# Kernel tuning notes

Hardware: AMD Instinct MI355X
Metric: run time of the kernel (lower is better)

## Reference

```python
import jax, jax.numpy as jnp
import numpy as np

BER = 0.02          # ber_curve.ber_at(snr_db) evaluated at snr_db=10
BITS = 9            # ceil(log2(512)) for both coarse and fine codebooks
KC = 512
KF = 512
B, HC, WC, HF, WF, D = 64, 32, 32, 64, 64, 128


def _bitflip_channel(idx, u, bits, K):
    """Pack->bitflip->unpack->clip, vectorized.

    LSB-first packing of exactly bits-per-symbol means flipping bits of the
    packed byte stream == flipping each symbol's `bits` bits independently
    (flipped padding bits in the final byte are discarded by unpack).
    idx: [...] int32, u: [..., bits] float32 uniform(0,1).
    """
    shifts = jnp.arange(bits, dtype=jnp.int32)
    bitmat = (idx[..., None] >> shifts) & 1                       # [..., bits]
    flips = (u < BER).astype(jnp.int32)
    bitmat = jnp.bitwise_xor(bitmat, flips)
    rx = jnp.sum(bitmat << shifts, axis=-1)                       # [...]
    return jnp.clip(rx, 0, K - 1)


def setup_inputs() -> dict:
    key = jax.random.key(0)
    k1, k2, k3, k4, k5, k6 = jax.random.split(key, 6)
    return {
        "idx_c": jax.random.randint(k1, (B, HC, WC), 0, KC, dtype=jnp.int32),
        "idx_f": jax.random.randint(k2, (B, HF, WF), 0, KF, dtype=jnp.int32),
        "codebook_c": jax.random.normal(k3, (KC, D), dtype=jnp.float32),
        "codebook_f": jax.random.normal(k4, (KF, D), dtype=jnp.float32),
        "flip_u_c": jax.random.uniform(k5, (B, HC, WC, BITS), dtype=jnp.float32),
        "flip_u_f": jax.random.uniform(k6, (B, HF, WF, BITS), dtype=jnp.float32),
    }


def reference(idx_c, idx_f, codebook_c, codebook_f, flip_u_c, flip_u_f):
    rx_c = _bitflip_channel(idx_c, flip_u_c, BITS, KC)            # [B,Hc,Wc]
    rx_f = _bitflip_channel(idx_f, flip_u_f, BITS, KF)            # [B,Hf,Wf]
    # indices_to_quantized: embedding gather from each codebook
    q_coarse = codebook_c[rx_c]                                   # [B,Hc,Wc,D]
    q_fine = codebook_f[rx_f]                                     # [B,Hf,Wf,D]
    b = q_fine.shape[0]
    out = jnp.concatenate(
        [q_fine.reshape(b, -1), q_coarse.reshape(b, -1)], axis=1
    )
    return out
```

## Files before the change

kernel.cpp:

```cpp
#include <hip/hip_runtime.h>


constexpr int   BITS       = 9;
constexpr float BER        = 0.02f;
constexpr int   Bn         = 64;
constexpr int   HC = 32, WC = 32, HF = 64, WF = 64, D = 128;
constexpr int   NF         = Bn * HF * WF;
constexpr int   NC         = Bn * HC * WC;
constexpr int   NTOT       = NF + NC;
constexpr int   FINE_ROW   = HF * WF * D;
constexpr int   COARSE_ROW = HC * WC * D;
constexpr int   ROW        = FINE_ROW + COARSE_ROW;

__global__ __launch_bounds__(256) void flip_kernel(
    const int*   __restrict__ idx_c,
    const int*   __restrict__ idx_f,
    const float* __restrict__ u_c,
    const float* __restrict__ u_f,
    int*         __restrict__ rx)
{
    const int s = blockIdx.x * 256 + threadIdx.x;
    const float* u;  const int* idxp;  int local;
    if (s < NF) { u = u_f; idxp = idx_f; local = s; }
    else        { u = u_c; idxp = idx_c; local = s - NF; }
    const float* up = u + (size_t)local * BITS;
    int flip = 0;
    #pragma unroll
    for (int k = 0; k < BITS; ++k)
        flip |= (up[k] < BER) ? (1 << k) : 0;
    rx[s] = (idxp[local] ^ flip) & 511;
}

constexpr int GRID  = 2048;
constexpr int ITERS = NTOT / (8 * GRID);

__global__ __launch_bounds__(256) void gather_kernel(
    const float* __restrict__ cb_c,
    const float* __restrict__ cb_f,
    const int*   __restrict__ rx,
    float*       __restrict__ out)
{
    const int t          = threadIdx.x;
    const int sym_in_blk = t >> 5;
    const int lane32     = t & 31;

    #pragma unroll 2
    for (int it = 0; it < ITERS; ++it) {
        const int i = (it * GRID + blockIdx.x) * 8 + sym_in_blk;
        const int row = rx[i];

        const float* cb;  int off;
        if (i < NF) {
            const int b = i >> 12, rem = i & 4095;
            off = b * ROW + rem * D;                cb = cb_f;
        } else {
            const int j = i - NF;
            const int b = j >> 10, rem = j & 1023;
            off = b * ROW + FINE_ROW + rem * D;     cb = cb_c;
        }

        const float4 val = ((const float4*)(cb + row * D))[lane32];
        ((float4*)(out + off))[lane32] = val;
    }
}

extern "C" void kernel_launch(void* const* d_in, const int* in_sizes, int n_in,
                              void* d_out, int out_size, void* d_ws, size_t ws_size,
                              hipStream_t stream) {
    const int*   idx_c = (const int*)  d_in[0];
    const int*   idx_f = (const int*)  d_in[1];
    const float* cb_c  = (const float*)d_in[2];
    const float* cb_f  = (const float*)d_in[3];
    const float* u_c   = (const float*)d_in[4];
    const float* u_f   = (const float*)d_in[5];
    float*       out   = (float*)d_out;
    int*         rx    = (int*)d_ws;

    flip_kernel<<<NTOT / 256, 256, 0, stream>>>(idx_c, idx_f, u_c, u_f, rx);
    gather_kernel<<<GRID, 256, 0, stream>>>(cb_c, cb_f, rx, out);
}
```

Before: 184.5 us.

## Fuse bit-flip channel and codebook gather into one kernel via shared memory

Merges the flip kernel and the gather kernel into a single launch. Each block computes received indices and output offsets for its contiguous 160 symbols into shared memory, then gathers codebook rows. This removes the second kernel launch and the global round trip of the rx workspace. The cost is that only 160 of 256 threads do the flip phase before a barrier, so the strided u loads sit on the critical path of every block.

```diff
diff --git a/kernel.cpp b/kernel.cpp
--- a/kernel.cpp
+++ b/kernel.cpp
@@ -12,55 +12,60 @@
 constexpr int   COARSE_ROW = HC * WC * D;
 constexpr int   ROW        = FINE_ROW + COARSE_ROW;
 
-__global__ __launch_bounds__(256) void flip_kernel(
+constexpr int   GRID       = 2048;
+constexpr int   SPB        = NTOT / GRID;
+constexpr int   P2_ITERS   = SPB / 8;
+
+__global__ __launch_bounds__(256) void fused_chan_gather(
     const int*   __restrict__ idx_c,
     const int*   __restrict__ idx_f,
+    const float* __restrict__ cb_c,
+    const float* __restrict__ cb_f,
     const float* __restrict__ u_c,
     const float* __restrict__ u_f,
-    int*         __restrict__ rx)
-{
-    const int s = blockIdx.x * 256 + threadIdx.x;
-    const float* u;  const int* idxp;  int local;
-    if (s < NF) { u = u_f; idxp = idx_f; local = s; }
-    else        { u = u_c; idxp = idx_c; local = s - NF; }
-    const float* up = u + (size_t)local * BITS;
-    int flip = 0;
-    #pragma unroll
-    for (int k = 0; k < BITS; ++k)
-        flip |= (up[k] < BER) ? (1 << k) : 0;
-    rx[s] = (idxp[local] ^ flip) & 511;
-}
-
-constexpr int GRID  = 2048;
-constexpr int ITERS = NTOT / (8 * GRID);
-
-__global__ __launch_bounds__(256) void gather_kernel(
-    const float* __restrict__ cb_c,
-    const float* __restrict__ cb_f,
-    const int*   __restrict__ rx,
     float*       __restrict__ out)
 {
-    const int t          = threadIdx.x;
-    const int sym_in_blk = t >> 5;
-    const int lane32     = t & 31;
+    __shared__ int s_row[SPB];
+    __shared__ int s_off[SPB];
+    __shared__ int s_crs[SPB];
 
-    #pragma unroll 2
-    for (int it = 0; it < ITERS; ++it) {
-        const int i = (it * GRID + blockIdx.x) * 8 + sym_in_blk;
-        const int row = rx[i];
+    const int t    = threadIdx.x;
+    const int base = blockIdx.x * SPB;
 
-        const float* cb;  int off;
+    if (t < SPB) {
+        const int i = base + t;
+        const float* u;  const int* idxp;  int local, off, crs;
         if (i < NF) {
+            local = i;
             const int b = i >> 12, rem = i & 4095;
-            off = b * ROW + rem * D;                cb = cb_f;
+            off = b * ROW + rem * D;
+            u = u_f;  idxp = idx_f;  crs = 0;
         } else {
-            const int j = i - NF;
-            const int b = j >> 10, rem = j & 1023;
-            off = b * ROW + FINE_ROW + rem * D;     cb = cb_c;
+            local = i - NF;
+            const int b = local >> 10, rem = local & 1023;
+            off = b * ROW + FINE_ROW + rem * D;
+            u = u_c;  idxp = idx_c;  crs = 1;
         }
+        const float* up = u + (size_t)local * BITS;
+        int flip = 0;
+        #pragma unroll
+        for (int k = 0; k < BITS; ++k)
+            flip |= (up[k] < BER) ? (1 << k) : 0;
+        s_row[t] = (idxp[local] ^ flip) & 511;
+        s_off[t] = off;
+        s_crs[t] = crs;
+    }
+    __syncthreads();
 
-        const float4 val = ((const float4*)(cb + row * D))[lane32];
-        ((float4*)(out + off))[lane32] = val;
+    const int g0     = t >> 5;
+    const int lane32 = t & 31;
+
+    #pragma unroll 4
+    for (int it = 0; it < P2_ITERS; ++it) {
+        const int sl  = it * 8 + g0;
+        const float* cb = s_crs[sl] ? cb_c : cb_f;
+        const float4 val = ((const float4*)(cb + s_row[sl] * D))[lane32];
+        ((float4*)(out + s_off[sl]))[lane32] = val;
     }
 }
 
@@ -74,8 +79,7 @@
     const float* u_c   = (const float*)d_in[4];
     const float* u_f   = (const float*)d_in[5];
     float*       out   = (float*)d_out;
-    int*         rx    = (int*)d_ws;
 
-    flip_kernel<<<NTOT / 256, 256, 0, stream>>>(idx_c, idx_f, u_c, u_f, rx);
-    gather_kernel<<<GRID, 256, 0, stream>>>(cb_c, cb_f, rx, out);
+    fused_chan_gather<<<GRID, 256, 0, stream>>>(
+        idx_c, idx_f, cb_c, cb_f, u_c, u_f, out);
 }
```

Result: no change. 184.6 us (+0.0%).
